# Kernel optimization log

Measured on AMD Instinct MI355X. Metric: run time of the kernel, lower is better.

Reference implementation:

```python
import jax, jax.numpy as jnp
import numpy as np
import math

B, S, D, H = 2, 2048, 512, 8
DK = D // H


def setup_inputs() -> dict:
    key = jax.random.key(0)
    ks = jax.random.split(key, 8)
    scale = 1.0 / math.sqrt(D)
    inp = {
        "query": jax.random.normal(ks[0], (B, S, D), dtype=jnp.float32),
        "key": jax.random.normal(ks[1], (B, S, D), dtype=jnp.float32),
        "value": jax.random.normal(ks[2], (B, S, D), dtype=jnp.float32),
        # causal mask, broadcast over batch and heads; masked_fill where mask == 0
        "mask": jnp.tril(jnp.ones((S, S), dtype=jnp.int32))[None, None, :, :],
        # nn.Linear(d_model, d_model, bias=False) weights, shape [out, in]
        "Wq": jax.random.uniform(ks[3], (D, D), jnp.float32, -scale, scale),
        "Wk": jax.random.uniform(ks[4], (D, D), jnp.float32, -scale, scale),
        "Wv": jax.random.uniform(ks[5], (D, D), jnp.float32, -scale, scale),
        "Wo": jax.random.uniform(ks[6], (D, D), jnp.float32, -scale, scale),
    }
    return inp


def reference(query, key, value, mask, Wq, Wk, Wv, Wo):
    b, s, d = query.shape
    h, dk = H, d // H
    q = query @ Wq.T                      # [B,S,D]
    _k_dead = key @ Wk.T                  # computed then discarded by the repo bug
    v = value @ Wv.T                      # [B,S,D]
    # raw .view() head split (NOT transpose-based) — faithful to the source
    qh = q.reshape(b, h, s, dk)           # [B,H,S,dk]
    kh = qh                               # repo bug: key = query.view(...)
    vh = v.reshape(b, h, s, dk)
    scores = jnp.einsum("bhqd,bhkd->bhqk", qh, kh) / math.sqrt(dk)  # [B,H,S,S]
    scores = jnp.where(mask == 0, jnp.float32(-1e9), scores)
    attn = jax.nn.softmax(scores, axis=-1)  # dropout p=0.0 -> identity
    x = jnp.einsum("bhqk,bhkd->bhqd", attn, vh)  # [B,H,S,dk]
    x = x.transpose(0, 2, 1, 3).reshape(b, s, h * dk)  # [B,S,D]
    return x @ Wo.T
```

## Files before the change

### kernel.cpp

```cpp
#include <hip/hip_runtime.h>


typedef unsigned short u16;
typedef unsigned int   u32;
typedef __attribute__((ext_vector_type(4))) float f32x4;
typedef __attribute__((ext_vector_type(8))) short bf16x8;
typedef __attribute__((ext_vector_type(4))) u16   us4;
typedef __attribute__((ext_vector_type(8))) u16   us8;

#define DEV static __device__ __forceinline__

DEV u16 f2b(float x) {
  union { float f; u32 u; } a; a.f = x;
  u32 u = a.u;
  u += 0x7fffu + ((u >> 16) & 1u);
  return (u16)(u >> 16);
}
DEV float b2f(u16 x) { union { u32 u; float f; } a; a.u = (u32)x << 16; return a.f; }
DEV us4 f4tob(f32x4 v) {
  us4 r; r[0] = f2b(v[0]); r[1] = f2b(v[1]); r[2] = f2b(v[2]); r[3] = f2b(v[3]);
  return r;
}

DEV u32 cvtpk(float lo, float hi) {
  u32 d;
  asm("v_cvt_pk_bf16_f32 %0, %1, %2" : "=v"(d) : "v"(lo), "v"(hi));
  return d;
}
DEV void swap32(u32& a, u32& b) {
  asm("v_permlane32_swap_b32 %0, %1" : "+v"(a), "+v"(b));
}
DEV void swap16(u32& a, u32& b) {
  asm("v_permlane16_swap_b32 %0, %1" : "+v"(a), "+v"(b));
}
DEV void swap32f(float& a, float& b) {
  asm("v_permlane32_swap_b32 %0, %1" : "+v"(a), "+v"(b));
}
DEV void swap16f(float& a, float& b) {
  asm("v_permlane16_swap_b32 %0, %1" : "+v"(a), "+v"(b));
}

DEV void gload16(const u16* g, u16* l) {
  __builtin_amdgcn_global_load_lds(
      (const __attribute__((address_space(1))) void*)(const void*)g,
      (__attribute__((address_space(3))) void*)(void*)l, 16, 0, 0);
}

constexpr int Kg = 512, Ng = 512;
constexpr int LDB = 136;

template<typename TA, int EPI>
DEV void gemm_body(const TA* __restrict__ A, const float* __restrict__ Bw,
                   void* __restrict__ outp, int bidx,
                   u16* __restrict__ sA, u16* __restrict__ sB) {
  const int tid  = threadIdx.x;
  const int lane = tid & 63;
  const int wid  = tid >> 6;
  const int bm   = bidx >> 3;
  const int bn   = bidx & 7;
  const int row0 = bm * 64, col0 = bn * 64;
  const int l16 = lane & 15, lhi = lane >> 4;
  const int wr = (wid >> 1) * 32, wc = (wid & 1) * 32;

  f32x4 acc[2][2];
#pragma unroll
  for (int mf = 0; mf < 2; ++mf)
#pragma unroll
    for (int nf = 0; nf < 2; ++nf) acc[mf][nf] = (f32x4)0.f;

  f32x4 ra[8];
  us8   ha[4];
  f32x4 rb[8];

  auto load_slab = [&](int kt) {
    if constexpr (sizeof(TA) == 4) {
#pragma unroll
      for (int i = 0; i < 8; ++i) {
        int id = tid + (i << 8); int r = id >> 5; int c = (id & 31) << 2;
        ra[i] = *reinterpret_cast<const f32x4*>(&A[(size_t)(row0 + r) * Kg + kt + c]);
      }
    } else {
#pragma unroll
      for (int i = 0; i < 4; ++i) {
        int id = tid + (i << 8); int r = id >> 4; int c = (id & 15) << 3;
        ha[i] = *reinterpret_cast<const us8*>(&A[(size_t)(row0 + r) * Kg + kt + c]);
      }
    }
#pragma unroll
    for (int i = 0; i < 8; ++i) {
      int id = tid + (i << 8); int r = id >> 5; int c = (id & 31) << 2;
      rb[i] = *reinterpret_cast<const f32x4*>(&Bw[(size_t)(col0 + r) * Kg + kt + c]);
    }
  };
  auto store_slab = [&]() {
    if constexpr (sizeof(TA) == 4) {
#pragma unroll
      for (int i = 0; i < 8; ++i) {
        int id = tid + (i << 8); int r = id >> 5; int c = (id & 31) << 2;
        *reinterpret_cast<us4*>(&sA[r * LDB + c]) = f4tob(ra[i]);
      }
    } else {
#pragma unroll
      for (int i = 0; i < 4; ++i) {
        int id = tid + (i << 8); int r = id >> 4; int c = (id & 15) << 3;
        *reinterpret_cast<us8*>(&sA[r * LDB + c]) = ha[i];
      }
    }
#pragma unroll
    for (int i = 0; i < 8; ++i) {
      int id = tid + (i << 8); int r = id >> 5; int c = (id & 31) << 2;
      *reinterpret_cast<us4*>(&sB[r * LDB + c]) = f4tob(rb[i]);
    }
  };

  load_slab(0);
  for (int kt = 0; kt < Kg; kt += 128) {
    __syncthreads();
    store_slab();
    __syncthreads();
    if (kt + 128 < Kg) load_slab(kt + 128);
    __builtin_amdgcn_s_setprio(1);
#pragma unroll
    for (int ks = 0; ks < 4; ++ks) {
      bf16x8 af[2], bv[2];
#pragma unroll
      for (int mf = 0; mf < 2; ++mf)
        af[mf] = *reinterpret_cast<const bf16x8*>(&sA[(wr + mf * 16 + l16) * LDB + ks * 32 + lhi * 8]);
#pragma unroll
      for (int nf = 0; nf < 2; ++nf)
        bv[nf] = *reinterpret_cast<const bf16x8*>(&sB[(wc + nf * 16 + l16) * LDB + ks * 32 + lhi * 8]);
#pragma unroll
      for (int mf = 0; mf < 2; ++mf)
#pragma unroll
        for (int nf = 0; nf < 2; ++nf)
          acc[mf][nf] = __builtin_amdgcn_mfma_f32_16x16x32_bf16(af[mf], bv[nf], acc[mf][nf], 0, 0, 0);
    }
    __builtin_amdgcn_s_setprio(0);
  }

#pragma unroll
  for (int mf = 0; mf < 2; ++mf)
#pragma unroll
    for (int nf = 0; nf < 2; ++nf)
#pragma unroll
      for (int r = 0; r < 4; ++r) {
        int grow = row0 + wr + mf * 16 + lhi * 4 + r;
        int gcol = col0 + wc + nf * 16 + l16;
        float v = acc[mf][nf][r];
        if constexpr (EPI == 0) {
          ((u16*)outp)[(size_t)grow * Ng + gcol] = f2b(v);
        } else if constexpr (EPI == 1) {
          int b = grow >> 11, srow = grow & 2047;
          int h = srow >> 8;
          int ss = ((srow & 255) << 3) + (gcol >> 6);
          int dd = gcol & 63;
          ((u16*)outp)[(((size_t)(b * 8 + h) * 64 + dd) << 11) + ss] = f2b(v);
        } else {
          ((float*)outp)[(size_t)grow * Ng + gcol] = v;
        }
      }
}

__global__ __launch_bounds__(256)
void qv_gemm_kernel(const float* __restrict__ query, const float* __restrict__ Wq,
                    const float* __restrict__ value, const float* __restrict__ Wv,
                    u16* __restrict__ qbf, u16* __restrict__ vt) {
  __shared__ u16 sA[64 * LDB];
  __shared__ u16 sB[64 * LDB];
  if (blockIdx.x < 512) gemm_body<float, 0>(query, Wq, qbf, blockIdx.x, sA, sB);
  else                  gemm_body<float, 1>(value, Wv, vt,  blockIdx.x - 512, sA, sB);
}

__global__ __launch_bounds__(256)
void o_gemm_kernel(const u16* __restrict__ opre, const float* __restrict__ Wo,
                   float* __restrict__ out) {
  __shared__ u16 sA[64 * LDB];
  __shared__ u16 sB[64 * LDB];
  gemm_body<u16, 2>(opre, Wo, out, blockIdx.x, sA, sB);
}

constexpr float SCL = 0.125f * 1.44269504088896340736f;
constexpr int NSPLIT = 4;

__global__ __launch_bounds__(256)
void attn_kernel(const u16* __restrict__ qbf, const u16* __restrict__ vt,
                 u16* __restrict__ opart, float* __restrict__ lsum) {
  __shared__ u16 sK[2][4096];
  __shared__ u16 sV[2][4096];
  const int tid  = threadIdx.x;
  const int lane = tid & 63;
  const int w    = tid >> 6;
  const int xcd  = blockIdx.x & 7;
  const int i    = blockIdx.x >> 3;
  const int qb   = 31 - (i >> 3);
  const int r8   = i & 7;
  const int bh   = 2 * xcd + (r8 >> 2);
  const int split = r8 & 3;
  const int q0 = qb * 64 + w * 16;
  const int l16 = lane & 15, lhi = lane >> 4;

  const u16* Qh = qbf + (size_t)bh * (2048 * 64);
  const u16* Vh = vt  + (size_t)bh * (64 * 2048);

  bf16x8 qf[2];
#pragma unroll
  for (int ks = 0; ks < 2; ++ks) {
    union { bf16x8 v; u32 wd[4]; } qw;
    qw.v = *reinterpret_cast<const bf16x8*>(&Qh[(q0 + l16) * 64 + ks * 32 + lhi * 8]);
#pragma unroll
    for (int j = 0; j < 4; ++j) {
      u32 u = qw.wd[j];
      float lo = b2f((u16)(u & 0xffffu)) * SCL;
      float hi = b2f((u16)(u >> 16)) * SCL;
      qw.wd[j] = cvtpk(lo, hi);
    }
    qf[ks] = qw.v;
  }

  f32x4 Oa[4];
#pragma unroll
  for (int nf = 0; nf < 4; ++nf) Oa[nf] = (f32x4)0.f;
  float rs = 0.f;

  const int ntiles = qb + 1;
  const int base = ntiles >> 2, rem = ntiles & 3;
  const int t0 = split * base + (split < rem ? split : rem);
  const int t1 = t0 + base + (split < rem ? 1 : 0);

  auto stage = [&](int buf, int t) {
    const int kb = t * 64;
#pragma unroll
    for (int j = 0; j < 2; ++j) {
      int u0 = w * 128 + j * 64;
      int u  = u0 + lane;
      int r  = u >> 3;
      int s  = (u & 7) ^ (r & 7);
      gload16(Qh + (size_t)(kb + r) * 64 + s * 8, &sK[buf][u0 * 8]);
      gload16(Vh + (size_t)r * 2048 + kb + s * 8, &sV[buf][u0 * 8]);
    }
  };

  if (t0 < t1) {
    stage(t0 & 1, t0);
    for (int kt = t0; kt < t1; ++kt) {
      __syncthreads();
      if (kt + 1 < t1) stage((kt + 1) & 1, kt + 1);
      const int kb = kt * 64;
      const u16* Kl = sK[kt & 1];
      const u16* Vl = sV[kt & 1];
      bf16x8 kf[8], vf[8];
#pragma unroll
      for (int nf = 0; nf < 4; ++nf)
#pragma unroll
        for (int ks = 0; ks < 2; ++ks) {
          int off = (nf * 16 + l16) * 64 + (((ks * 4 + lhi) ^ (l16 & 7)) * 8);
          kf[nf * 2 + ks] = *reinterpret_cast<const bf16x8*>(&Kl[off]);
          vf[nf * 2 + ks] = *reinterpret_cast<const bf16x8*>(&Vl[off]);
        }
      f32x4 s[4];
#pragma unroll
      for (int nf = 0; nf < 4; ++nf) s[nf] = (f32x4)0.f;
      __builtin_amdgcn_s_setprio(1);
#pragma unroll
      for (int nf = 0; nf < 4; ++nf)
#pragma unroll
        for (int ks = 0; ks < 2; ++ks)
          s[nf] = __builtin_amdgcn_mfma_f32_16x16x32_bf16(kf[nf * 2 + ks], qf[ks], s[nf], 0, 0, 0);
      __builtin_amdgcn_s_setprio(0);
      if (kb + 63 > q0) {
        const int row = q0 + l16;
#pragma unroll
        for (int nf = 0; nf < 4; ++nf)
#pragma unroll
          for (int r = 0; r < 4; ++r) {
            int col = kb + nf * 16 + lhi * 4 + r;
            if (col > row) s[nf][r] = -1e30f;
          }
      }
#pragma unroll
      for (int nf = 0; nf < 4; ++nf)
#pragma unroll
        for (int r = 0; r < 4; ++r) {
          float p = exp2f(s[nf][r]);
          s[nf][r] = p;
          rs += p;
        }
      u32 pk[4][2];
#pragma unroll
      for (int nf = 0; nf < 4; ++nf)
#pragma unroll
        for (int rr = 0; rr < 2; ++rr)
          pk[nf][rr] = cvtpk(s[nf][2 * rr], s[nf][2 * rr + 1]);
      union { u32 wd[4]; bf16x8 v; } pa[2];
#pragma unroll
      for (int ks = 0; ks < 2; ++ks)
#pragma unroll
        for (int rr = 0; rr < 2; ++rr) {
          u32 X = pk[2 * ks][rr], Y = pk[2 * ks + 1][rr];
          swap32(X, Y);
          swap16(X, Y);
          pa[ks].wd[rr]     = X;
          pa[ks].wd[2 + rr] = Y;
        }
      __builtin_amdgcn_s_setprio(1);
#pragma unroll
      for (int nf = 0; nf < 4; ++nf)
#pragma unroll
        for (int ks = 0; ks < 2; ++ks)
          Oa[nf] = __builtin_amdgcn_mfma_f32_16x16x32_bf16(pa[ks].v, vf[nf * 2 + ks], Oa[nf], 0, 0, 0);
      __builtin_amdgcn_s_setprio(0);
    }
  }

  {
    float a = rs, b = rs;
    swap16f(a, b);
    float y = a + b;
    float c = y, d = y;
    swap32f(c, d);
    rs = c + d;
  }

  u16* op = opart + ((size_t)split * 32768 + bh * 2048) * 64;
#pragma unroll
  for (int nf = 0; nf < 4; ++nf)
#pragma unroll
    for (int r = 0; r < 4; ++r) {
      int row = q0 + lhi * 4 + r;
      op[(size_t)row * 64 + nf * 16 + l16] = f2b(Oa[nf][r]);
    }
  if (lane < 16)
    lsum[(size_t)split * 32768 + bh * 2048 + q0 + lane] = rs;
}

__global__ __launch_bounds__(256)
void merge_kernel(const u16* __restrict__ opart, const float* __restrict__ lsum,
                  u16* __restrict__ opre) {
  const int gid = blockIdx.x * 256 + threadIdx.x;
  const int row = gid >> 3;
  const int c   = gid & 7;
  float den = 0.f;
#pragma unroll
  for (int s = 0; s < NSPLIT; ++s) den += lsum[(size_t)s * 32768 + row];
  const float inv = 1.f / den;
  float acc[8];
#pragma unroll
  for (int j = 0; j < 8; ++j) acc[j] = 0.f;
#pragma unroll
  for (int s = 0; s < NSPLIT; ++s) {
    us8 o = *reinterpret_cast<const us8*>(&opart[((size_t)s * 32768 + row) * 64 + c * 8]);
#pragma unroll
    for (int j = 0; j < 8; ++j) acc[j] += b2f(o[j]);
  }
  us8 o;
#pragma unroll
  for (int j = 0; j < 8; ++j) o[j] = f2b(acc[j] * inv);
  const int bh = row >> 11, srow = row & 2047;
  const int b = bh >> 3, h = bh & 7;
  *reinterpret_cast<us8*>(&opre[((size_t)b * 2048 + srow) * 512 + h * 64 + c * 8]) = o;
}

extern "C" void kernel_launch(void* const* d_in, const int* in_sizes, int n_in,
                              void* d_out, int out_size, void* d_ws, size_t ws_size,
                              hipStream_t stream) {
  const float* query = (const float*)d_in[0];
  const float* value = (const float*)d_in[2];
  const float* Wq = (const float*)d_in[4];
  const float* Wv = (const float*)d_in[6];
  const float* Wo = (const float*)d_in[7];

  u16* qbf   = (u16*)d_ws;
  u16* vt    = qbf + 2097152;
  u16* opre  = vt + 2097152;
  u16* opart = opre + 2097152;
  float* lsum = (float*)(opart + NSPLIT * 2097152);
  float* out = (float*)d_out;

  qv_gemm_kernel<<<dim3(1024), dim3(256), 0, stream>>>(query, Wq, value, Wv, qbf, vt);
  attn_kernel<<<dim3(2048), dim3(256), 0, stream>>>(qbf, vt, opart, lsum);
  merge_kernel<<<dim3(1024), dim3(256), 0, stream>>>(opart, lsum, opre);
  o_gemm_kernel<<<dim3(512), dim3(256), 0, stream>>>(opre, Wo, out);
}
```

Baseline: 74.01 us.

## Pre-convert GEMM operands to bf16 and use async LDS loads with swizzle

```diff
diff --git a/kernel.cpp b/kernel.cpp
--- a/kernel.cpp
+++ b/kernel.cpp
@@ -46,21 +46,38 @@
       (__attribute__((address_space(3))) void*)(void*)l, 16, 0, 0);
 }
 
-constexpr int Kg = 512, Ng = 512;
-constexpr int LDB = 136;
-
-template<typename TA, int EPI>
-DEV void gemm_body(const TA* __restrict__ A, const float* __restrict__ Bw,
-                   void* __restrict__ outp, int bidx,
-                   u16* __restrict__ sA, u16* __restrict__ sB) {
+__global__ __launch_bounds__(256)
+void cvt_kernel(const float* __restrict__ q, const float* __restrict__ v,
+                const float* __restrict__ wq, const float* __restrict__ wv,
+                const float* __restrict__ wo,
+                u16* __restrict__ aq, u16* __restrict__ av,
+                u16* __restrict__ bq, u16* __restrict__ bv, u16* __restrict__ bo) {
+  int cid = blockIdx.x * 256 + threadIdx.x;
+  const float* src; u16* dst; int off;
+  if      (cid < 262144) { src = q;  dst = aq; off = cid; }
+  else if (cid < 524288) { src = v;  dst = av; off = cid - 262144; }
+  else if (cid < 557056) { src = wq; dst = bq; off = cid - 524288; }
+  else if (cid < 589824) { src = wv; dst = bv; off = cid - 557056; }
+  else                   { src = wo; dst = bo; off = cid - 589824; }
+  f32x4 a = *reinterpret_cast<const f32x4*>(src + (size_t)off * 8);
+  f32x4 b = *reinterpret_cast<const f32x4*>(src + (size_t)off * 8 + 4);
+  us4 lo = f4tob(a), hi = f4tob(b);
+  us8 o;
+  o[0] = lo[0]; o[1] = lo[1]; o[2] = lo[2]; o[3] = lo[3];
+  o[4] = hi[0]; o[5] = hi[1]; o[6] = hi[2]; o[7] = hi[3];
+  *reinterpret_cast<us8*>(dst + (size_t)off * 8) = o;
+}
+
+template<int EPI>
+DEV void gemm_fast_body(const u16* __restrict__ A, const u16* __restrict__ Bw,
+                        void* __restrict__ outp, int bm, int bn,
+                        u16* __restrict__ sA, u16* __restrict__ sB) {
   const int tid  = threadIdx.x;
   const int lane = tid & 63;
-  const int wid  = tid >> 6;
-  const int bm   = bidx >> 3;
-  const int bn   = bidx & 7;
+  const int w    = tid >> 6;
   const int row0 = bm * 64, col0 = bn * 64;
   const int l16 = lane & 15, lhi = lane >> 4;
-  const int wr = (wid >> 1) * 32, wc = (wid & 1) * 32;
+  const int wr = (w >> 1) * 32, wc = (w & 1) * 32;
 
   f32x4 acc[2][2];
 #pragma unroll
@@ -68,67 +85,38 @@
 #pragma unroll
     for (int nf = 0; nf < 2; ++nf) acc[mf][nf] = (f32x4)0.f;
 
-  f32x4 ra[8];
-  us8   ha[4];
-  f32x4 rb[8];
-
-  auto load_slab = [&](int kt) {
-    if constexpr (sizeof(TA) == 4) {
-#pragma unroll
-      for (int i = 0; i < 8; ++i) {
-        int id = tid + (i << 8); int r = id >> 5; int c = (id & 31) << 2;
-        ra[i] = *reinterpret_cast<const f32x4*>(&A[(size_t)(row0 + r) * Kg + kt + c]);
+  auto stage = [&](int buf, int kt) {
+#pragma unroll
+    for (int i = 0; i < 2; ++i) {
+      int u0 = w * 128 + i * 64;
+      int u  = u0 + lane;
+      int r  = u >> 3;
+      int s  = (u & 7) ^ (r & 7);
+      gload16(A  + (size_t)(row0 + r) * 512 + kt + s * 8, &sA[buf * 4096 + u0 * 8]);
+      gload16(Bw + (size_t)(col0 + r) * 512 + kt + s * 8, &sB[buf * 4096 + u0 * 8]);
+    }
+  };
+
+  stage(0, 0);
+  for (int t = 0; t < 8; ++t) {
+    __syncthreads();
+    if (t + 1 < 8) stage((t + 1) & 1, (t + 1) * 64);
+    const u16* Ka = &sA[(t & 1) * 4096];
+    const u16* Kb = &sB[(t & 1) * 4096];
+    __builtin_amdgcn_s_setprio(1);
+#pragma unroll
+    for (int ks = 0; ks < 2; ++ks) {
+      bf16x8 af[2], bv[2];
+#pragma unroll
+      for (int mf = 0; mf < 2; ++mf) {
+        int unit = (ks * 4 + lhi) ^ (l16 & 7);
+        af[mf] = *reinterpret_cast<const bf16x8*>(&Ka[(wr + mf * 16 + l16) * 64 + unit * 8]);
       }
-    } else {
-#pragma unroll
-      for (int i = 0; i < 4; ++i) {
-        int id = tid + (i << 8); int r = id >> 4; int c = (id & 15) << 3;
-        ha[i] = *reinterpret_cast<const us8*>(&A[(size_t)(row0 + r) * Kg + kt + c]);
+#pragma unroll
+      for (int nf = 0; nf < 2; ++nf) {
+        int unit = (ks * 4 + lhi) ^ (l16 & 7);
+        bv[nf] = *reinterpret_cast<const bf16x8*>(&Kb[(wc + nf * 16 + l16) * 64 + unit * 8]);
       }
-    }
-#pragma unroll
-    for (int i = 0; i < 8; ++i) {
-      int id = tid + (i << 8); int r = id >> 5; int c = (id & 31) << 2;
-      rb[i] = *reinterpret_cast<const f32x4*>(&Bw[(size_t)(col0 + r) * Kg + kt + c]);
-    }
-  };
-  auto store_slab = [&]() {
-    if constexpr (sizeof(TA) == 4) {
-#pragma unroll
-      for (int i = 0; i < 8; ++i) {
-        int id = tid + (i << 8); int r = id >> 5; int c = (id & 31) << 2;
-        *reinterpret_cast<us4*>(&sA[r * LDB + c]) = f4tob(ra[i]);
-      }
-    } else {
-#pragma unroll
-      for (int i = 0; i < 4; ++i) {
-        int id = tid + (i << 8); int r = id >> 4; int c = (id & 15) << 3;
-        *reinterpret_cast<us8*>(&sA[r * LDB + c]) = ha[i];
-      }
-    }
-#pragma unroll
-    for (int i = 0; i < 8; ++i) {
-      int id = tid + (i << 8); int r = id >> 5; int c = (id & 31) << 2;
-      *reinterpret_cast<us4*>(&sB[r * LDB + c]) = f4tob(rb[i]);
-    }
-  };
-
-  load_slab(0);
-  for (int kt = 0; kt < Kg; kt += 128) {
-    __syncthreads();
-    store_slab();
-    __syncthreads();
-    if (kt + 128 < Kg) load_slab(kt + 128);
-    __builtin_amdgcn_s_setprio(1);
-#pragma unroll
-    for (int ks = 0; ks < 4; ++ks) {
-      bf16x8 af[2], bv[2];
-#pragma unroll
-      for (int mf = 0; mf < 2; ++mf)
-        af[mf] = *reinterpret_cast<const bf16x8*>(&sA[(wr + mf * 16 + l16) * LDB + ks * 32 + lhi * 8]);
-#pragma unroll
-      for (int nf = 0; nf < 2; ++nf)
-        bv[nf] = *reinterpret_cast<const bf16x8*>(&sB[(wc + nf * 16 + l16) * LDB + ks * 32 + lhi * 8]);
 #pragma unroll
       for (int mf = 0; mf < 2; ++mf)
 #pragma unroll
@@ -148,7 +136,7 @@
         int gcol = col0 + wc + nf * 16 + l16;
         float v = acc[mf][nf][r];
         if constexpr (EPI == 0) {
-          ((u16*)outp)[(size_t)grow * Ng + gcol] = f2b(v);
+          ((u16*)outp)[(size_t)grow * 512 + gcol] = f2b(v);
         } else if constexpr (EPI == 1) {
           int b = grow >> 11, srow = grow & 2047;
           int h = srow >> 8;
@@ -156,27 +144,34 @@
           int dd = gcol & 63;
           ((u16*)outp)[(((size_t)(b * 8 + h) * 64 + dd) << 11) + ss] = f2b(v);
         } else {
-          ((float*)outp)[(size_t)grow * Ng + gcol] = v;
+          ((float*)outp)[(size_t)grow * 512 + gcol] = v;
         }
       }
 }
 
 __global__ __launch_bounds__(256)
-void qv_gemm_kernel(const float* __restrict__ query, const float* __restrict__ Wq,
-                    const float* __restrict__ value, const float* __restrict__ Wv,
+void qv_gemm_kernel(const u16* __restrict__ aq, const u16* __restrict__ av,
+                    const u16* __restrict__ wqb, const u16* __restrict__ wvb,
                     u16* __restrict__ qbf, u16* __restrict__ vt) {
-  __shared__ u16 sA[64 * LDB];
-  __shared__ u16 sB[64 * LDB];
-  if (blockIdx.x < 512) gemm_body<float, 0>(query, Wq, qbf, blockIdx.x, sA, sB);
-  else                  gemm_body<float, 1>(value, Wv, vt,  blockIdx.x - 512, sA, sB);
-}
-
-__global__ __launch_bounds__(256)
-void o_gemm_kernel(const u16* __restrict__ opre, const float* __restrict__ Wo,
+  __shared__ u16 sA[2 * 4096];
+  __shared__ u16 sB[2 * 4096];
+  const int xcd = blockIdx.x & 7;
+  const int local = blockIdx.x >> 3;
+  const int g = local >> 6, rem = local & 63;
+  const int bm = xcd * 8 + (rem >> 3), bn = rem & 7;
+  if (g == 0) gemm_fast_body<0>(aq, wqb, qbf, bm, bn, sA, sB);
+  else        gemm_fast_body<1>(av, wvb, vt,  bm, bn, sA, sB);
+}
+
+__global__ __launch_bounds__(256)
+void o_gemm_kernel(const u16* __restrict__ opre, const u16* __restrict__ wob,
                    float* __restrict__ out) {
-  __shared__ u16 sA[64 * LDB];
-  __shared__ u16 sB[64 * LDB];
-  gemm_body<u16, 2>(opre, Wo, out, blockIdx.x, sA, sB);
+  __shared__ u16 sA[2 * 4096];
+  __shared__ u16 sB[2 * 4096];
+  const int xcd = blockIdx.x & 7;
+  const int local = blockIdx.x >> 3;
+  const int bm = xcd * 8 + (local >> 3), bn = local & 7;
+  gemm_fast_body<2>(opre, wob, out, bm, bn, sA, sB);
 }
 
 constexpr float SCL = 0.125f * 1.44269504088896340736f;
@@ -373,11 +368,18 @@
   u16* vt    = qbf + 2097152;
   u16* opre  = vt + 2097152;
   u16* opart = opre + 2097152;
-  float* lsum = (float*)(opart + NSPLIT * 2097152);
+  u16* aq    = opart + NSPLIT * 2097152;
+  u16* av    = aq + 2097152;
+  u16* wqb   = av + 2097152;
+  u16* wvb   = wqb + 262144;
+  u16* wob   = wvb + 262144;
+  float* lsum = (float*)(wob + 262144);
   float* out = (float*)d_out;
 
-  qv_gemm_kernel<<<dim3(1024), dim3(256), 0, stream>>>(query, Wq, value, Wv, qbf, vt);
+  cvt_kernel<<<dim3(2432), dim3(256), 0, stream>>>(query, value, Wq, Wv, Wo,
+                                                   aq, av, wqb, wvb, wob);
+  qv_gemm_kernel<<<dim3(1024), dim3(256), 0, stream>>>(aq, av, wqb, wvb, qbf, vt);
   attn_kernel<<<dim3(2048), dim3(256), 0, stream>>>(qbf, vt, opart, lsum);
   merge_kernel<<<dim3(1024), dim3(256), 0, stream>>>(opart, lsum, opre);
-  o_gemm_kernel<<<dim3(512), dim3(256), 0, stream>>>(opre, Wo, out);
-}
+  o_gemm_kernel<<<dim3(512), dim3(256), 0, stream>>>(opre, wob, out);
+}
```

Measured after the change: 60.81 us. -17.8%, faster.
